# Kernel optimization log

Measured on AMD Instinct MI355X. Metric: run time of the kernel, lower is better.

The kernel has to match this reference:

```python
import jax, jax.numpy as jnp
import numpy as np
from jax import lax

B, H, W, CIN, COUT, K, SDIM = 8, 256, 256, 128, 128, 3, 512


def setup_inputs() -> dict:
    key = jax.random.key(0)
    k1, k2, k3, k4, k5 = jax.random.split(key, 5)
    return {
        "x": jax.random.normal(k1, (B, H, W, CIN), dtype=jnp.float32),
        "style": jax.random.normal(k2, (B, SDIM), dtype=jnp.float32),
        "kernel": jax.random.normal(k3, (K, K, CIN, COUT), dtype=jnp.float32),
        "w_mod": jax.random.normal(k4, (SDIM, CIN), dtype=jnp.float32) / np.sqrt(SDIM),
        "b_mod": jnp.zeros((CIN,), dtype=jnp.float32),
        "noise_strength": jnp.zeros((1,), dtype=jnp.float32),
        "bias": jnp.zeros((COUT,), dtype=jnp.float32),
        "noise": jax.random.normal(k5, (B, H, W, 1), dtype=jnp.float32),
    }


def reference(x, style, kernel, w_mod, b_mod, noise_strength, bias, noise):
    kh, kw, cin, cout = kernel.shape
    # equalized-lr runtime coefficient
    he_std = 1.0 / jnp.sqrt(jnp.asarray(kh * kw * cin, jnp.float32))
    w = kernel * he_std  # [kh,kw,cin,cout]
    # style modulation (Dense with zero constant bias) + 1
    s = style @ w_mod + b_mod + 1.0  # [B, cin]
    # demodulate=True: normalize by global max-abs of style (as in source)
    s = s * (1.0 / jnp.max(jnp.abs(s)))
    # NOTE: source uses style[0] only -> single shared modulated weight
    w = w * s[0][None, None, :, None]
    d = lax.rsqrt(jnp.sum(jnp.square(w), axis=(0, 1, 2)) + 1e-8)  # [cout]
    w = w * d[None, None, None, :]
    # plain conv branch: NHWC, stride 1, SAME padding
    y = lax.conv_general_dilated(
        x, w, window_strides=(1, 1), padding="SAME",
        dimension_numbers=("NHWC", "HWIO", "NHWC"))
    # noise injection (noise_strength is zero-init, kept for faithfulness)
    y = y + noise * (noise_strength / 2.0)
    y = y + bias
    # lrelu(0.2) * sqrt(2)
    y = jnp.where(y >= 0, y, 0.2 * y) * jnp.sqrt(jnp.asarray(2.0, y.dtype))
    return y
```

## Files before the change

kernel.cpp:

```cpp
#include <hip/hip_runtime.h>
#include <hip/hip_bf16.h>

#define H 256
#define W 256
#define CIN 128
#define COUT 128
#define BATCH 8
#define LDA 136

typedef float f32x4 __attribute__((ext_vector_type(4)));
typedef short bf16x8 __attribute__((ext_vector_type(8)));

static __device__ __forceinline__ unsigned short f2bf(float f) {
    unsigned int x = __float_as_uint(f);
    unsigned int r = (x + 0x7fffu + ((x >> 16) & 1u)) >> 16;
    return (unsigned short)r;
}

__device__ float g_s0[CIN];
__device__ float g_bmax[BATCH];
__device__ float g_partial[9 * COUT];

__global__ __launch_bounds__(256) void mod_style(
    const float* __restrict__ style, const float* __restrict__ w_mod,
    const float* __restrict__ b_mod)
{
    __shared__ float red[256];
    const int t = threadIdx.x;
    const int b = blockIdx.x;
    const int c = t & 127;
    const int half = t >> 7;

    float acc = 0.f;
    const float4* st4 = (const float4*)(style + b * 512 + half * 256);
    const float* wm = w_mod + half * 256 * CIN + c;
    for (int k4 = 0; k4 < 64; ++k4) {
        float4 s4 = st4[k4];
        const float* w = wm + k4 * 4 * CIN;
        acc += s4.x * w[0 * CIN];
        acc += s4.y * w[1 * CIN];
        acc += s4.z * w[2 * CIN];
        acc += s4.w * w[3 * CIN];
    }
    red[t] = acc;
    __syncthreads();
    if (t < 128) {
        float sval = red[t] + red[t + 128] + b_mod[t] + 1.0f;
        if (b == 0) g_s0[t] = sval;
        red[t] = fabsf(sval);
    }
    __syncthreads();
    for (int off = 64; off > 0; off >>= 1) {
        if (t < off) red[t] = fmaxf(red[t], red[t + off]);
        __syncthreads();
    }
    if (t == 0) g_bmax[b] = red[0];
}

__global__ __launch_bounds__(256) void demod_partial(
    const float* __restrict__ kern)
{
    __shared__ float scale[CIN];
    __shared__ float red[256];
    const int t = threadIdx.x;
    const int kk = blockIdx.x;
    const int co = t & 127;
    const int half = t >> 7;

    if (t < 128) {
        float m = g_bmax[0];
        #pragma unroll
        for (int i = 1; i < BATCH; ++i) m = fmaxf(m, g_bmax[i]);
        const float he_std = 1.0f / sqrtf(1152.0f);
        scale[t] = g_s0[t] * (1.0f / m) * he_std;
    }
    __syncthreads();

    float ss = 0.f;
    const float* kbase = kern + (size_t)kk * 128 * 128 + co;
    for (int j = 0; j < 64; ++j) {
        int ci = half * 64 + j;
        float wv = kbase[(size_t)ci * 128] * scale[ci];
        ss += wv * wv;
    }
    red[t] = ss;
    __syncthreads();
    if (t < 128) g_partial[kk * 128 + t] = red[t] + red[t + 128];
}

__global__ __launch_bounds__(256) void swizzle_kernel(
    const float* __restrict__ kern, unsigned short* __restrict__ wprep)
{
    __shared__ float scale[CIN];
    __shared__ float dArr[COUT];
    const int t = threadIdx.x;
    const int u = blockIdx.x * 256 + t;

    if (t < 128) {
        float m = g_bmax[0];
        #pragma unroll
        for (int i = 1; i < BATCH; ++i) m = fmaxf(m, g_bmax[i]);
        const float he_std = 1.0f / sqrtf(1152.0f);
        scale[t] = g_s0[t] * (1.0f / m) * he_std;
        float sum = 0.f;
        #pragma unroll
        for (int g = 0; g < 9; ++g) sum += g_partial[g * 128 + t];
        dArr[t] = rsqrtf(sum + 1e-8f);
    }
    __syncthreads();

    const int lane  = u & 63;
    const int ntile = (u >> 6) & 7;
    const int kc    = (u >> 9) & 3;
    const int kk    = u >> 11;
    const int co  = ntile * 16 + (lane & 15);
    const int cib = kc * 32 + (lane >> 4) * 8;
    const float dv = dArr[co];
    unsigned int packed[4];
    #pragma unroll
    for (int jp = 0; jp < 4; ++jp) {
        int ci0 = cib + jp * 2;
        float w0 = kern[(kk * 128 + ci0)     * 128 + co] * scale[ci0]     * dv;
        float w1 = kern[(kk * 128 + ci0 + 1) * 128 + co] * scale[ci0 + 1] * dv;
        packed[jp] = (unsigned int)f2bf(w0) | ((unsigned int)f2bf(w1) << 16);
    }
    ((uint4*)wprep)[u] = make_uint4(packed[0], packed[1], packed[2], packed[3]);
}

__global__ __launch_bounds__(256) void conv_kernel(
    const float* __restrict__ x, const unsigned short* __restrict__ wprep,
    const float* __restrict__ noise_strength, const float* __restrict__ bias,
    const float* __restrict__ noise, float* __restrict__ out)
{
    __shared__ unsigned short ldsA[130 * LDA];
    const int tid  = threadIdx.x;
    const int lane = tid & 63;
    const int wave = tid >> 6;
    const int wm = wave & 1;
    const int wn = wave >> 1;
    const int wt = blockIdx.x;
    const int h  = blockIdx.y;
    const int b  = blockIdx.z;
    const int wstart = wt * 128;

    f32x4 acc[4][4];
    const f32x4 zero = {0.f, 0.f, 0.f, 0.f};
    for (int i = 0; i < 4; ++i)
        for (int j = 0; j < 4; ++j) acc[i][j] = zero;

    for (int kh = 0; kh < 3; ++kh) {
        __syncthreads();
        const int hImg = h + kh - 1;
        const bool rowValid = (hImg >= 0) && (hImg < H);
        const float* rowPtr = x + ((size_t)(b * H + hImg) * W) * CIN;
        for (int idx = tid; idx < 130 * 32; idx += 256) {
            int p  = idx >> 5;
            int c4 = idx & 31;
            int wImg = wstart - 1 + p;
            float4 v = make_float4(0.f, 0.f, 0.f, 0.f);
            if (rowValid && (unsigned)wImg < (unsigned)W)
                v = *(const float4*)(rowPtr + (size_t)wImg * CIN + c4 * 4);
            ushort4 u;
            u.x = f2bf(v.x); u.y = f2bf(v.y); u.z = f2bf(v.z); u.w = f2bf(v.w);
            *(ushort4*)&ldsA[p * LDA + c4 * 4] = u;
        }
        __syncthreads();

        #pragma unroll
        for (int kw = 0; kw < 3; ++kw) {
            const int kk = kh * 3 + kw;
            #pragma unroll
            for (int kc = 0; kc < 4; ++kc) {
                bf16x8 bfrag[4], afrag[4];
                const bf16x8* bptr = (const bf16x8*)wprep +
                                     (((kk * 4 + kc) * 8 + wn * 4) * 64 + lane);
                #pragma unroll
                for (int j = 0; j < 4; ++j) bfrag[j] = bptr[j * 64];
                const int ka = kc * 32 + (lane >> 4) * 8;
                #pragma unroll
                for (int i = 0; i < 4; ++i) {
                    int m = wm * 64 + i * 16 + (lane & 15) + kw;
                    afrag[i] = *(const bf16x8*)&ldsA[m * LDA + ka];
                }
                #pragma unroll
                for (int i = 0; i < 4; ++i)
                    #pragma unroll
                    for (int j = 0; j < 4; ++j)
                        acc[i][j] = __builtin_amdgcn_mfma_f32_16x16x32_bf16(
                            afrag[i], bfrag[j], acc[i][j], 0, 0, 0);
            }
        }
    }

    const float ns  = noise_strength[0] * 0.5f;
    const float RT2 = 1.41421356237309515f;
    const size_t pixBase = ((size_t)(b * H + h) * W) + wstart;
    #pragma unroll
    for (int i = 0; i < 4; ++i) {
        const int mbase = wm * 64 + i * 16 + ((lane >> 4) << 2);
        #pragma unroll
        for (int r = 0; r < 4; ++r) {
            const size_t pix = pixBase + (mbase + r);
            const float nz = noise[pix] * ns;
            #pragma unroll
            for (int j = 0; j < 4; ++j) {
                const int col = wn * 64 + j * 16 + (lane & 15);
                float v = acc[i][j][r] + nz + bias[col];
                v = (v >= 0.f ? v : 0.2f * v) * RT2;
                out[pix * COUT + col] = v;
            }
        }
    }
}

extern "C" void kernel_launch(void* const* d_in, const int* in_sizes, int n_in,
                              void* d_out, int out_size, void* d_ws, size_t ws_size,
                              hipStream_t stream) {
    const float* x              = (const float*)d_in[0];
    const float* style          = (const float*)d_in[1];
    const float* kern           = (const float*)d_in[2];
    const float* w_mod          = (const float*)d_in[3];
    const float* b_mod          = (const float*)d_in[4];
    const float* noise_strength = (const float*)d_in[5];
    const float* bias           = (const float*)d_in[6];
    const float* noise          = (const float*)d_in[7];
    float* out = (float*)d_out;
    unsigned short* wprep = (unsigned short*)d_ws;

    hipLaunchKernelGGL(mod_style, dim3(8), dim3(256), 0, stream,
                       style, w_mod, b_mod);
    hipLaunchKernelGGL(demod_partial, dim3(9), dim3(256), 0, stream, kern);
    hipLaunchKernelGGL(swizzle_kernel, dim3(72), dim3(256), 0, stream,
                       kern, wprep);
    hipLaunchKernelGGL(conv_kernel, dim3(2, 256, 8), dim3(256), 0, stream,
                       x, wprep, noise_strength, bias, noise, out);
}
```

Baseline: 700.2 us.

## Double-buffer input rows in LDS and prefetch weight fragments in conv

The conv kernel now keeps two LDS row buffers. The next input row is loaded from global memory into registers while MFMAs run on the current row, and it is written to LDS afterwards. Weight B-fragments are software-pipelined two steps ahead in a ping-pong register buffer, and launch bounds now request two blocks per CU. This aims to hide global-load latency behind compute, at the cost of doubled LDS use and 17 float4 staging registers, which may cause spills or lower occupancy.

```diff
diff --git a/kernel.cpp b/kernel.cpp
--- a/kernel.cpp
+++ b/kernel.cpp
@@ -127,12 +127,78 @@
     ((uint4*)wprep)[u] = make_uint4(packed[0], packed[1], packed[2], packed[3]);
 }
 
-__global__ __launch_bounds__(256) void conv_kernel(
+static __device__ __forceinline__ void issue_row(
+    float4 (&st)[17], const float* __restrict__ x, int b, int hImg,
+    int wstart, int tid)
+{
+    const bool rv = ((unsigned)hImg < (unsigned)H);
+    const float* rp = x + ((size_t)(b * H + hImg) * W) * CIN;
+    #pragma unroll
+    for (int k = 0; k < 17; ++k) {
+        const int idx = tid + k * 256;
+        st[k] = make_float4(0.f, 0.f, 0.f, 0.f);
+        if (k < 16 || tid < 64) {
+            const int p  = idx >> 5;
+            const int c4 = idx & 31;
+            const int wImg = wstart - 1 + p;
+            if (rv && (unsigned)wImg < (unsigned)W)
+                st[k] = *(const float4*)(rp + (size_t)wImg * CIN + c4 * 4);
+        }
+    }
+}
+
+static __device__ __forceinline__ void write_row(
+    const float4 (&st)[17], unsigned short* __restrict__ buf, int tid)
+{
+    #pragma unroll
+    for (int k = 0; k < 17; ++k) {
+        const int idx = tid + k * 256;
+        if (k < 16 || tid < 64) {
+            const int p  = idx >> 5;
+            const int c4 = idx & 31;
+            ushort4 u;
+            u.x = f2bf(st[k].x); u.y = f2bf(st[k].y);
+            u.z = f2bf(st[k].z); u.w = f2bf(st[k].w);
+            *(ushort4*)&buf[p * LDA + c4 * 4] = u;
+        }
+    }
+}
+
+template<int KH>
+static __device__ __forceinline__ void compute_kh(
+    const unsigned short* __restrict__ slot,
+    const bf16x8* __restrict__ bb,
+    bf16x8 (&bp)[2][4], f32x4 (&acc)[4][4], const int lane, const int wm)
+{
+    #pragma unroll
+    for (int kw = 0; kw < 3; ++kw) {
+        #pragma unroll
+        for (int kc = 0; kc < 4; ++kc) {
+            const int p   = KH * 12 + kw * 4 + kc;
+            const int sel = p & 1;
+            const int ka  = kc * 32 + (lane >> 4) * 8;
+            #pragma unroll
+            for (int i = 0; i < 4; ++i) {
+                const int m = wm * 64 + i * 16 + (lane & 15) + kw;
+                bf16x8 af = *(const bf16x8*)&slot[m * LDA + ka];
+                #pragma unroll
+                for (int j = 0; j < 4; ++j)
+                    acc[i][j] = __builtin_amdgcn_mfma_f32_16x16x32_bf16(
+                        af, bp[sel][j], acc[i][j], 0, 0, 0);
+            }
+            const int gn = (p + 2 < 36) ? p + 2 : p + 2 - 36;
+            #pragma unroll
+            for (int j = 0; j < 4; ++j) bp[sel][j] = bb[gn * 512 + j * 64];
+        }
+    }
+}
+
+__global__ __launch_bounds__(256, 2) void conv_kernel(
     const float* __restrict__ x, const unsigned short* __restrict__ wprep,
     const float* __restrict__ noise_strength, const float* __restrict__ bias,
     const float* __restrict__ noise, float* __restrict__ out)
 {
-    __shared__ unsigned short ldsA[130 * LDA];
+    __shared__ unsigned short ldsA[2][130 * LDA];
     const int tid  = threadIdx.x;
     const int lane = tid & 63;
     const int wave = tid >> 6;
@@ -144,53 +210,35 @@
     const int wstart = wt * 128;
 
     f32x4 acc[4][4];
-    const f32x4 zero = {0.f, 0.f, 0.f, 0.f};
+    #pragma unroll
     for (int i = 0; i < 4; ++i)
-        for (int j = 0; j < 4; ++j) acc[i][j] = zero;
-
-    for (int kh = 0; kh < 3; ++kh) {
-        __syncthreads();
-        const int hImg = h + kh - 1;
-        const bool rowValid = (hImg >= 0) && (hImg < H);
-        const float* rowPtr = x + ((size_t)(b * H + hImg) * W) * CIN;
-        for (int idx = tid; idx < 130 * 32; idx += 256) {
-            int p  = idx >> 5;
-            int c4 = idx & 31;
-            int wImg = wstart - 1 + p;
-            float4 v = make_float4(0.f, 0.f, 0.f, 0.f);
-            if (rowValid && (unsigned)wImg < (unsigned)W)
-                v = *(const float4*)(rowPtr + (size_t)wImg * CIN + c4 * 4);
-            ushort4 u;
-            u.x = f2bf(v.x); u.y = f2bf(v.y); u.z = f2bf(v.z); u.w = f2bf(v.w);
-            *(ushort4*)&ldsA[p * LDA + c4 * 4] = u;
-        }
-        __syncthreads();
-
-        #pragma unroll
-        for (int kw = 0; kw < 3; ++kw) {
-            const int kk = kh * 3 + kw;
-            #pragma unroll
-            for (int kc = 0; kc < 4; ++kc) {
-                bf16x8 bfrag[4], afrag[4];
-                const bf16x8* bptr = (const bf16x8*)wprep +
-                                     (((kk * 4 + kc) * 8 + wn * 4) * 64 + lane);
-                #pragma unroll
-                for (int j = 0; j < 4; ++j) bfrag[j] = bptr[j * 64];
-                const int ka = kc * 32 + (lane >> 4) * 8;
-                #pragma unroll
-                for (int i = 0; i < 4; ++i) {
-                    int m = wm * 64 + i * 16 + (lane & 15) + kw;
-                    afrag[i] = *(const bf16x8*)&ldsA[m * LDA + ka];
-                }
-                #pragma unroll
-                for (int i = 0; i < 4; ++i)
-                    #pragma unroll
-                    for (int j = 0; j < 4; ++j)
-                        acc[i][j] = __builtin_amdgcn_mfma_f32_16x16x32_bf16(
-                            afrag[i], bfrag[j], acc[i][j], 0, 0, 0);
-            }
-        }
-    }
+        #pragma unroll
+        for (int j = 0; j < 4; ++j) acc[i][j] = (f32x4){0.f, 0.f, 0.f, 0.f};
+
+    const bf16x8* bb = (const bf16x8*)wprep + wn * 256 + lane;
+    bf16x8 bp[2][4];
+    #pragma unroll
+    for (int j = 0; j < 4; ++j) bp[0][j] = bb[j * 64];
+    #pragma unroll
+    for (int j = 0; j < 4; ++j) bp[1][j] = bb[512 + j * 64];
+
+    float4 st[17];
+
+    issue_row(st, x, b, h - 1, wstart, tid);
+    write_row(st, ldsA[0], tid);
+    issue_row(st, x, b, h, wstart, tid);
+    __syncthreads();
+
+    compute_kh<0>(ldsA[0], bb, bp, acc, lane, wm);
+    write_row(st, ldsA[1], tid);
+    issue_row(st, x, b, h + 1, wstart, tid);
+    __syncthreads();
+
+    compute_kh<1>(ldsA[1], bb, bp, acc, lane, wm);
+    write_row(st, ldsA[0], tid);
+    __syncthreads();
+
+    compute_kh<2>(ldsA[0], bb, bp, acc, lane, wm);
 
     const float ns  = noise_strength[0] * 0.5f;
     const float RT2 = 1.41421356237309515f;
```

Measured after the change: 625.8 us. 10.6% less time.
